# Kernel tuning notes

Hardware: AMD Instinct MI355X
Metric: run time of the kernel (lower is better)

## Reference

```python
import jax, jax.numpy as jnp
import numpy as np

N = 50000      # nodes
E = 400000     # edges (before self-loops)
IN = 128       # input feature dim
HID = 32       # out_channels per head
HEADS = 12
NC = 2         # num_classes
SLOPE = 0.2    # GATv2 leaky_relu negative slope


def setup_inputs() -> dict:
    key = jax.random.key(0)
    ks = jax.random.split(key, 24)
    f32 = jnp.float32
    def nrm(k, shape, s=0.1):
        return jax.random.normal(k, shape, dtype=f32) * s
    inp = {}
    inp["x"] = jax.random.normal(ks[0], (N, IN), dtype=f32)
    inp["edge_index"] = jax.random.randint(ks[1], (2, E), 0, N, dtype=jnp.int32)
    # GATv2 layer 0: in=IN, layer 1: in=HID; both heads=HEADS, out=HID, concat=False
    dims = [IN, HID]
    i = 2
    for l, d in enumerate(dims):
        inp[f"Wl{l}"] = nrm(ks[i], (d, HEADS * HID)); i += 1
        inp[f"bl{l}"] = jnp.zeros((HEADS * HID,), f32)
        inp[f"Wr{l}"] = nrm(ks[i], (d, HEADS * HID)); i += 1
        inp[f"br{l}"] = jnp.zeros((HEADS * HID,), f32)
        inp[f"att{l}"] = nrm(ks[i], (HEADS, HID)); i += 1
        inp[f"bias{l}"] = jnp.zeros((HID,), f32)
    # output GATv2Conv(HID, NC): heads=1, concat=True
    inp["Wlo"] = nrm(ks[i], (HID, NC)); i += 1
    inp["blo"] = jnp.zeros((NC,), f32)
    inp["Wro"] = nrm(ks[i], (HID, NC)); i += 1
    inp["bro"] = jnp.zeros((NC,), f32)
    inp["atto"] = nrm(ks[i], (1, NC)); i += 1
    inp["biaso"] = jnp.zeros((NC,), f32)
    return inp


def gatv2_conv(x, src, dst, Wl, bl, Wr, br, att, bias, heads, out_ch, concat):
    """PyG GATv2Conv (share_weights=False, self-loops pre-appended, eval mode)."""
    n = x.shape[0]
    xl = (x @ Wl + bl).reshape(n, heads, out_ch)   # source transform
    xr = (x @ Wr + br).reshape(n, heads, out_ch)   # target transform
    # per-edge attention: e_ij = att . leaky_relu(xl_j + xr_i)
    h = jax.nn.leaky_relu(xl[src] + xr[dst], SLOPE)            # [E, H, C]
    logits = jnp.einsum('ehc,hc->eh', h, att)                   # [E, H]
    # segment softmax over incoming edges per destination node
    m = jax.ops.segment_max(logits, dst, num_segments=n)        # [N, H]
    a = jnp.exp(logits - m[dst])
    denom = jax.ops.segment_sum(a, dst, num_segments=n)         # [N, H]
    alpha = a / (denom[dst] + 1e-16)                            # [E, H]
    out = jax.ops.segment_sum(xl[src] * alpha[..., None], dst, num_segments=n)
    out = out.reshape(n, heads * out_ch) if concat else out.mean(axis=1)
    return out + bias


def reference(x, edge_index, Wl0, bl0, Wr0, br0, att0, bias0,
              Wl1, bl1, Wr1, br1, att1, bias1,
              Wlo, blo, Wro, bro, atto, biaso):
    n = x.shape[0]
    loop = jnp.arange(n, dtype=edge_index.dtype)
    src = jnp.concatenate([edge_index[0], loop])  # add self-loops (PyG default)
    dst = jnp.concatenate([edge_index[1], loop])
    h = gatv2_conv(x, src, dst, Wl0, bl0, Wr0, br0, att0, bias0, HEADS, HID, False)
    h = jax.nn.elu(h)
    h = gatv2_conv(h, src, dst, Wl1, bl1, Wr1, br1, att1, bias1, HEADS, HID, False)
    h = jax.nn.elu(h)
    out = gatv2_conv(h, src, dst, Wlo, blo, Wro, bro, atto, biaso, 1, NC, True)
    return out
```

## Files before the change

kernel.cpp:

```cpp
#include <hip/hip_runtime.h>
#include <hip/hip_fp16.h>
#include <math.h>

#define IN_DIM 128
#define HID 32
#define HEADS 12
#define FDIM (HEADS*HID)
#define SLOPE 0.2f

typedef __attribute__((ext_vector_type(8))) short short8;
typedef __attribute__((ext_vector_type(4))) float float4v;
typedef __attribute__((ext_vector_type(4))) float f32x4;
typedef _Float16 hv2 __attribute__((ext_vector_type(2)));

__device__ __forceinline__ float dot2acc(hv2 a, hv2 b, float c) {
#if __has_builtin(__builtin_amdgcn_fdot2)
    return __builtin_amdgcn_fdot2(a, b, c, false);
#else
    return c + (float)a.x * (float)b.x + (float)a.y * (float)b.y;
#endif
}


__global__ void hist_kernel(const int* __restrict__ dst, int* __restrict__ cnt, int E) {
    int e = blockIdx.x * blockDim.x + threadIdx.x;
    if (e < E) atomicAdd(&cnt[dst[e]], 1);
}

__global__ __launch_bounds__(256) void scan_partial_kernel(const int* __restrict__ cnt,
                                                           int* __restrict__ partials, int n) {
    int i = blockIdx.x * 256 + threadIdx.x;
    int v = (i < n) ? cnt[i] : 0;
#pragma unroll
    for (int off = 1; off < 64; off <<= 1) v += __shfl_xor(v, off);
    __shared__ int sh[4];
    if ((threadIdx.x & 63) == 0) sh[threadIdx.x >> 6] = v;
    __syncthreads();
    if (threadIdx.x == 0) partials[blockIdx.x] = sh[0] + sh[1] + sh[2] + sh[3];
}

__global__ __launch_bounds__(1024) void scan_top_kernel(int* __restrict__ partials, int nb) {
    __shared__ int sh[1024];
    int t = threadIdx.x;
    int v = (t < nb) ? partials[t] : 0;
    sh[t] = v;
    __syncthreads();
    for (int off = 1; off < 1024; off <<= 1) {
        int u = (t >= off) ? sh[t - off] : 0;
        __syncthreads();
        sh[t] += u;
        __syncthreads();
    }
    if (t < nb) partials[t] = sh[t] - v;
}

__global__ __launch_bounds__(256) void scan_final_kernel(const int* __restrict__ cnt,
                                                         const int* __restrict__ partials,
                                                         int* __restrict__ start,
                                                         int* __restrict__ cursor, int n) {
    __shared__ int sh[256];
    int t = threadIdx.x;
    int i = blockIdx.x * 256 + t;
    int v = (i < n) ? cnt[i] : 0;
    sh[t] = v;
    __syncthreads();
    for (int off = 1; off < 256; off <<= 1) {
        int u = (t >= off) ? sh[t - off] : 0;
        __syncthreads();
        sh[t] += u;
        __syncthreads();
    }
    int ex = sh[t] - v + partials[blockIdx.x];
    if (i < n) {
        start[i] = ex;
        cursor[i] = ex;
        if (i == n - 1) start[n] = ex + v;
    }
}

__global__ void scatter_kernel(const int* __restrict__ src, const int* __restrict__ dst,
                               int* __restrict__ cursor, int* __restrict__ srcs,
                               int* __restrict__ srcsOff, int E) {
    int e = blockIdx.x * blockDim.x + threadIdx.x;
    if (e < E) {
        int d = dst[e];
        int pos = atomicAdd(&cursor[d], 1);
        int s = src[e];
        srcs[pos] = s;
        srcsOff[pos] = s * (FDIM * 2);
    }
}


__device__ __forceinline__ unsigned int bf16_rne(float f) {
    unsigned int u = __float_as_uint(f);
    return (u + 0x7FFFu + ((u >> 16) & 1u)) >> 16;
}


__global__ void prep_all(const float* __restrict__ Wl0, const float* __restrict__ Wr0,
                         const float* __restrict__ Wl1, const float* __restrict__ Wr1,
                         const float* __restrict__ a0, const float* __restrict__ a1,
                         short* __restrict__ Bl0h, short* __restrict__ Bl0l,
                         short* __restrict__ Br0h, short* __restrict__ Br0l,
                         short* __restrict__ Bl1h, short* __restrict__ Bl1l,
                         short* __restrict__ Br1h, short* __restrict__ Br1l,
                         _Float16* __restrict__ attH) {
    int idx = blockIdx.x * 256 + threadIdx.x;
    if (idx < 49152) {
        int k = idx / 384, n = idx - k * 384;
        float w1 = Wl0[idx], w2 = Wr0[idx];
        unsigned int h1 = bf16_rne(w1);
        unsigned int l1 = bf16_rne(w1 - __uint_as_float(h1 << 16));
        unsigned int h2 = bf16_rne(w2);
        unsigned int l2 = bf16_rne(w2 - __uint_as_float(h2 << 16));
        Bl0h[n * 128 + k] = (short)h1;  Bl0l[n * 128 + k] = (short)l1;
        Br0h[n * 128 + k] = (short)h2;  Br0l[n * 128 + k] = (short)l2;
    } else if (idx < 61440) {
        int i2 = idx - 49152;
        int k = i2 / 384, n = i2 - k * 384;
        float w1 = Wl1[i2], w2 = Wr1[i2];
        unsigned int h1 = bf16_rne(w1);
        unsigned int l1 = bf16_rne(w1 - __uint_as_float(h1 << 16));
        unsigned int h2 = bf16_rne(w2);
        unsigned int l2 = bf16_rne(w2 - __uint_as_float(h2 << 16));
        Bl1h[n * 32 + k] = (short)h1;  Bl1l[n * 32 + k] = (short)l1;
        Br1h[n * 32 + k] = (short)h2;  Br1l[n * 32 + k] = (short)l2;
    } else if (idx < 62208) {
        int i2 = idx - 61440;
        attH[i2] = (_Float16)((i2 < 384) ? a0[i2] : a1[i2 - 384]);
    }
}


__global__ void conv_x_kernel(const float* __restrict__ A, short* __restrict__ Ah,
                              short* __restrict__ Al, int total4) {
    int i = blockIdx.x * 256 + threadIdx.x;
    if (i >= total4) return;
    float4 v = ((const float4*)A)[i];
    float fs[4] = {v.x, v.y, v.z, v.w};
    unsigned int hb[4], lb[4];
#pragma unroll
    for (int t = 0; t < 4; t++) {
        hb[t] = bf16_rne(fs[t]);
        lb[t] = bf16_rne(fs[t] - __uint_as_float(hb[t] << 16));
    }
    uint2 hp, lp;
    hp.x = hb[0] | (hb[1] << 16); hp.y = hb[2] | (hb[3] << 16);
    lp.x = lb[0] | (lb[1] << 16); lp.y = lb[2] | (lb[3] << 16);
    ((uint2*)Ah)[i] = hp;
    ((uint2*)Al)[i] = lp;
}


__global__ __launch_bounds__(256) void gemm_pair_direct(
    const short* __restrict__ Ahi, const short* __restrict__ Alo,
    const short* __restrict__ B1h, const short* __restrict__ B1l,
    const float* __restrict__ bias1, __half* __restrict__ C1,
    const short* __restrict__ B2h, const short* __restrict__ B2l,
    const float* __restrict__ bias2, __half* __restrict__ C2,
    int M, int K) {
    __shared__ __align__(16) float Ct[64 * 132];
    int tid = threadIdx.x;
    int lane = tid & 63;
    int wave = tid >> 6;
    int wm = wave & 1, wn = wave >> 1;
    int rowBase = blockIdx.x * 128;
    bool second = blockIdx.y >= 3;
    int colBase = (blockIdx.y - (second ? 3 : 0)) * 128;
    const short* Bh  = second ? B2h : B1h;
    const short* Bl  = second ? B2l : B1l;
    const float* bias = second ? bias2 : bias1;
    __half*      C    = second ? C2 : C1;

    int fr = lane & 15;
    int fo = (lane >> 4) << 3;

    float4v acc[4][4];
#pragma unroll
    for (int i = 0; i < 4; i++)
#pragma unroll
        for (int j = 0; j < 4; j++) acc[i][j] = (float4v){0.f, 0.f, 0.f, 0.f};

    const short* Ar = Ahi + (long)(rowBase + wm * 64 + fr) * K + fo;
    const short* Al_ = Alo + (long)(rowBase + wm * 64 + fr) * K + fo;
    const short* Br_ = Bh + (long)(colBase + wn * 64 + fr) * K + fo;
    const short* Bl_ = Bl + (long)(colBase + wn * 64 + fr) * K + fo;
    long rstep = (long)16 * K;

    for (int kt = 0; kt < K; kt += 32) {
        short8 ah[4], al[4], bh[4], blv[4];
#pragma unroll
        for (int i = 0; i < 4; i++) {
            ah[i]  = *(const short8*)(Ar  + i * rstep + kt);
            al[i]  = *(const short8*)(Al_ + i * rstep + kt);
            bh[i]  = *(const short8*)(Br_ + i * rstep + kt);
            blv[i] = *(const short8*)(Bl_ + i * rstep + kt);
        }
#pragma unroll
        for (int i = 0; i < 4; i++)
#pragma unroll
            for (int j = 0; j < 4; j++) {
                acc[i][j] = __builtin_amdgcn_mfma_f32_16x16x32_bf16(ah[i], bh[j],  acc[i][j], 0, 0, 0);
                acc[i][j] = __builtin_amdgcn_mfma_f32_16x16x32_bf16(ah[i], blv[j], acc[i][j], 0, 0, 0);
                acc[i][j] = __builtin_amdgcn_mfma_f32_16x16x32_bf16(al[i], bh[j],  acc[i][j], 0, 0, 0);
            }
    }

    int cq = lane >> 4, cn = lane & 15;
#pragma unroll
    for (int ph = 0; ph < 2; ph++) {
        __syncthreads();
        if (wm == ph) {
#pragma unroll
            for (int i = 0; i < 4; i++)
#pragma unroll
                for (int j = 0; j < 4; j++) {
                    int lr = i * 16 + cq * 4;
                    int lc = wn * 64 + j * 16 + cn;
#pragma unroll
                    for (int r = 0; r < 4; r++)
                        Ct[(lr + r) * 132 + lc] = acc[i][j][r];
                }
        }
        __syncthreads();
#pragma unroll
        for (int k = 0; k < 4; k++) {
            int o = k * 256 + tid;
            int lr = o >> 4;
            int oc = (o & 15) << 3;
            int gr = rowBase + ph * 64 + lr;
            if (gr < M) {
                float4 f0 = *(float4*)&Ct[lr * 132 + oc];
                float4 f1 = *(float4*)&Ct[lr * 132 + oc + 4];
                int gc = colBase + oc;
                float4 b0 = *(const float4*)(bias + gc);
                float4 b1 = *(const float4*)(bias + gc + 4);
                __half2 p0 = __floats2half2_rn(f0.x + b0.x, f0.y + b0.y);
                __half2 p1 = __floats2half2_rn(f0.z + b0.z, f0.w + b0.w);
                __half2 p2 = __floats2half2_rn(f1.x + b1.x, f1.y + b1.y);
                __half2 p3 = __floats2half2_rn(f1.z + b1.z, f1.w + b1.w);
                uint4 ov;
                ov.x = *(unsigned int*)&p0;
                ov.y = *(unsigned int*)&p1;
                ov.z = *(unsigned int*)&p2;
                ov.w = *(unsigned int*)&p3;
                *(uint4*)(C + (size_t)gr * FDIM + gc) = ov;
            }
        }
    }
}


__global__ __launch_bounds__(64) void agg_kernel(const __half* __restrict__ xl,
                                                 const __half* __restrict__ xr,
                                                 const _Float16* __restrict__ att_h,
                                                 const float* __restrict__ bias,
                                                 const int* __restrict__ start,
                                                 const int* __restrict__ srcsOff,
                                                 short* __restrict__ houtHi,
                                                 short* __restrict__ houtLo,
                                                 const float* __restrict__ Wl,
                                                 const float* __restrict__ bl,
                                                 const float* __restrict__ Wr,
                                                 const float* __restrict__ br,
                                                 float* __restrict__ xloB,
                                                 float* __restrict__ xroB, int N) {
    int node = blockIdx.x;
    if (node >= N) return;
    int lane = threadIdx.x & 63;
    int hl = lane & 31;
    int half_ = lane >> 5;
    int cb = hl << 3;

    long nodeOff = (long)node * (FDIM * 2);
    hv2 xr2[6], at2[6];
    f32x4 acc[3];
    float s[3];
#pragma unroll
    for (int c = 0; c < 3; c++) {
        uint2 ur = *(const uint2*)((const char*)xr + nodeOff + c * 256 + cb);
        xr2[2*c]   = __builtin_bit_cast(hv2, ur.x);
        xr2[2*c+1] = __builtin_bit_cast(hv2, ur.y);
        uint2 ua = *(const uint2*)((const char*)att_h + c * 256 + cb);
        at2[2*c]   = __builtin_bit_cast(hv2, ua.x);
        at2[2*c+1] = __builtin_bit_cast(hv2, ua.y);
        acc[c] = (f32x4){0.f, 0.f, 0.f, 0.f};
        s[c] = 0.f;
    }
    const hv2 sl2 = {(_Float16)SLOPE, (_Float16)SLOPE};
    const char* xlb = (const char*)xl;

    int e0 = start[node], e1 = start[node + 1];

    for (int b = e0 - 1; b < e1; b += 4) {
        hv2 xa[2][6];
        float mask[2];
#pragma unroll
        for (int p = 0; p < 2; p++) {
            int myIdx = b + p * 2 + half_;
            int ic = min(myIdx, e1 - 1);
            long off = (ic < e0) ? nodeOff : (long)srcsOff[ic];
            mask[p] = (myIdx < e1) ? 0.f : -1e30f;
            const char* base = xlb + off + cb;
            uint2 u0 = *(const uint2*)(base);
            uint2 u1 = *(const uint2*)(base + 256);
            uint2 u2 = *(const uint2*)(base + 512);
            xa[p][0] = __builtin_bit_cast(hv2, u0.x); xa[p][1] = __builtin_bit_cast(hv2, u0.y);
            xa[p][2] = __builtin_bit_cast(hv2, u1.x); xa[p][3] = __builtin_bit_cast(hv2, u1.y);
            xa[p][4] = __builtin_bit_cast(hv2, u2.x); xa[p][5] = __builtin_bit_cast(hv2, u2.y);
        }
#pragma unroll
        for (int p = 0; p < 2; p++) {
            float pc[3];
#pragma unroll
            for (int c = 0; c < 3; c++) {
                hv2 t0 = xa[p][2*c]   + xr2[2*c];
                hv2 t1 = xa[p][2*c+1] + xr2[2*c+1];
                t0 = __builtin_elementwise_max(t0, t0 * sl2);
                t1 = __builtin_elementwise_max(t1, t1 * sl2);
                pc[c] = dot2acc(t1, at2[2*c+1], dot2acc(t0, at2[2*c], 0.f));
            }
#pragma unroll
            for (int st = 1; st <= 4; st <<= 1) {
                pc[0] += __shfl_xor(pc[0], st);
                pc[1] += __shfl_xor(pc[1], st);
                pc[2] += __shfl_xor(pc[2], st);
            }
#pragma unroll
            for (int c = 0; c < 3; c++) {
                float a = __expf(pc[c] + mask[p]);
                s[c] += a;
                acc[c].x = fmaf(a, (float)xa[p][2*c].x,   acc[c].x);
                acc[c].y = fmaf(a, (float)xa[p][2*c].y,   acc[c].y);
                acc[c].z = fmaf(a, (float)xa[p][2*c+1].x, acc[c].z);
                acc[c].w = fmaf(a, (float)xa[p][2*c+1].y, acc[c].w);
            }
        }
    }

#pragma unroll
    for (int c = 0; c < 3; c++) {
        acc[c].x += __shfl_xor(acc[c].x, 32);
        acc[c].y += __shfl_xor(acc[c].y, 32);
        acc[c].z += __shfl_xor(acc[c].z, 32);
        acc[c].w += __shfl_xor(acc[c].w, 32);
        s[c] += __shfl_xor(s[c], 32);
    }
    f32x4 v[3];
#pragma unroll
    for (int c = 0; c < 3; c++) {
        float inv = 1.f / (s[c] + 1e-16f);
        f32x4 iv = {inv, inv, inv, inv};
        v[c] = acc[c] * iv;
    }
#pragma unroll
    for (int st = 8; st <= 16; st <<= 1) {
#pragma unroll
        for (int c = 0; c < 3; c++) {
            v[c].x += __shfl_xor(v[c].x, st);
            v[c].y += __shfl_xor(v[c].y, st);
            v[c].z += __shfl_xor(v[c].z, st);
            v[c].w += __shfl_xor(v[c].w, st);
        }
    }
    if (lane < 8) {
        f32x4 b4 = *(const f32x4*)(bias + (hl << 2));
        f32x4 o = (v[0] + v[1] + v[2]) * (f32x4){1.f/12.f, 1.f/12.f, 1.f/12.f, 1.f/12.f} + b4;
        o.x = o.x > 0.f ? o.x : expm1f(o.x);
        o.y = o.y > 0.f ? o.y : expm1f(o.y);
        o.z = o.z > 0.f ? o.z : expm1f(o.z);
        o.w = o.w > 0.f ? o.w : expm1f(o.w);
        if (houtHi) {
            float fs[4] = {o.x, o.y, o.z, o.w};
            unsigned int hb[4], lb[4];
#pragma unroll
            for (int t = 0; t < 4; t++) {
                hb[t] = bf16_rne(fs[t]);
                lb[t] = bf16_rne(fs[t] - __uint_as_float(hb[t] << 16));
            }
            uint2 hp, lp;
            hp.x = hb[0] | (hb[1] << 16); hp.y = hb[2] | (hb[3] << 16);
            lp.x = lb[0] | (lb[1] << 16); lp.y = lb[2] | (lb[3] << 16);
            *(uint2*)(houtHi + (size_t)node * 32 + (hl << 2)) = hp;
            *(uint2*)(houtLo + (size_t)node * 32 + (hl << 2)) = lp;
        }
        if (Wl) {
            f32x4 wl0 = *(const f32x4*)(Wl + (hl << 3));
            f32x4 wl1 = *(const f32x4*)(Wl + (hl << 3) + 4);
            f32x4 wr0 = *(const f32x4*)(Wr + (hl << 3));
            f32x4 wr1 = *(const f32x4*)(Wr + (hl << 3) + 4);
            float l0 = o.x * wl0.x + o.y * wl0.z + o.z * wl1.x + o.w * wl1.z;
            float l1 = o.x * wl0.y + o.y * wl0.w + o.z * wl1.y + o.w * wl1.w;
            float r0 = o.x * wr0.x + o.y * wr0.z + o.z * wr1.x + o.w * wr1.z;
            float r1 = o.x * wr0.y + o.y * wr0.w + o.z * wr1.y + o.w * wr1.w;
#pragma unroll
            for (int st = 1; st <= 4; st <<= 1) {
                l0 += __shfl_xor(l0, st); l1 += __shfl_xor(l1, st);
                r0 += __shfl_xor(r0, st); r1 += __shfl_xor(r1, st);
            }
            if (hl == 0) {
                xloB[2 * node]     = l0 + bl[0];
                xloB[2 * node + 1] = l1 + bl[1];
                xroB[2 * node]     = r0 + br[0];
                xroB[2 * node + 1] = r1 + br[1];
            }
        }
    }
}


__global__ void out_agg_kernel(const float* __restrict__ xlo, const float* __restrict__ xro,
                               const float* __restrict__ atto, const float* __restrict__ biaso,
                               const int* __restrict__ start, const int* __restrict__ srcs,
                               float* __restrict__ out, int N) {
    int i = blockIdx.x * blockDim.x + threadIdx.x;
    if (i >= N) return;
    float a0 = atto[0], a1 = atto[1];
    float xr0 = xro[2 * i], xr1 = xro[2 * i + 1];
    float s = 0.f, acc0 = 0.f, acc1 = 0.f;
    int e0 = start[i], e1 = start[i + 1];
    for (int idx = e0 - 1; idx < e1; ++idx) {
        int j = (idx < e0) ? i : srcs[idx];
        float x0 = xlo[2 * j], x1 = xlo[2 * j + 1];
        float t0 = x0 + xr0, t1 = x1 + xr1;
        t0 = fmaxf(t0, SLOPE * t0);
        t1 = fmaxf(t1, SLOPE * t1);
        float L = a0 * t0 + a1 * t1;
        float a = __expf(L);
        s += a;
        acc0 = fmaf(a, x0, acc0);
        acc1 = fmaf(a, x1, acc1);
    }
    float inv = 1.0f / (s + 1e-16f);
    out[2 * i]     = acc0 * inv + biaso[0];
    out[2 * i + 1] = acc1 * inv + biaso[1];
}


extern "C" void kernel_launch(void* const* d_in, const int* in_sizes, int n_in,
                              void* d_out, int out_size, void* d_ws, size_t ws_size,
                              hipStream_t stream) {
    const float* x    = (const float*)d_in[0];
    const int*   ei   = (const int*)d_in[1];
    const float* Wl0  = (const float*)d_in[2];
    const float* bl0  = (const float*)d_in[3];
    const float* Wr0  = (const float*)d_in[4];
    const float* br0  = (const float*)d_in[5];
    const float* att0 = (const float*)d_in[6];
    const float* bias0= (const float*)d_in[7];
    const float* Wl1  = (const float*)d_in[8];
    const float* bl1  = (const float*)d_in[9];
    const float* Wr1  = (const float*)d_in[10];
    const float* br1  = (const float*)d_in[11];
    const float* att1 = (const float*)d_in[12];
    const float* bias1= (const float*)d_in[13];
    const float* Wlo  = (const float*)d_in[14];
    const float* blo  = (const float*)d_in[15];
    const float* Wro  = (const float*)d_in[16];
    const float* bro  = (const float*)d_in[17];
    const float* atto = (const float*)d_in[18];
    const float* biaso= (const float*)d_in[19];

    const int N = in_sizes[0] / IN_DIM;
    const int E = in_sizes[1] / 2;

    char* ws = (char*)d_ws;
    size_t off = 0;
    auto take = [&](size_t bytes) -> char* {
        char* p = ws + off;
        off += (bytes + 255) & ~(size_t)255;
        return p;
    };
    __half* xlf = (__half*)take((size_t)N * FDIM * 2);
    __half* xrf = (__half*)take((size_t)N * FDIM * 2);
    float* xloB = (float*)take((size_t)N * 2 * 4);
    float* xroB = (float*)take((size_t)N * 2 * 4);
    int* cnt    = (int*)take((size_t)N * 4);
    int* startA = (int*)take((size_t)(N + 1) * 4);
    int* cursor = (int*)take((size_t)N * 4);
    int* srcs   = (int*)take((size_t)E * 4);
    int* srcsOff= (int*)take((size_t)E * 4);
    int  nb     = (N + 255) / 256;
    int* partials = (int*)take((size_t)nb * 4);
    short* Bl0h = (short*)take((size_t)FDIM * IN_DIM * 2);
    short* Bl0l = (short*)take((size_t)FDIM * IN_DIM * 2);
    short* Br0h = (short*)take((size_t)FDIM * IN_DIM * 2);
    short* Br0l = (short*)take((size_t)FDIM * IN_DIM * 2);
    short* Bl1h = (short*)take((size_t)FDIM * HID * 2);
    short* Bl1l = (short*)take((size_t)FDIM * HID * 2);
    short* Br1h = (short*)take((size_t)FDIM * HID * 2);
    short* Br1l = (short*)take((size_t)FDIM * HID * 2);
    short* xh   = (short*)take((size_t)N * IN_DIM * 2);
    short* xlo_ = (short*)take((size_t)N * IN_DIM * 2);
    short* h0h  = (short*)take((size_t)N * HID * 2);
    short* h0l  = (short*)take((size_t)N * HID * 2);
    _Float16* attH = (_Float16*)take((size_t)768 * 2);
    (void)take(16384);

    const int* esrc = ei;
    const int* edst = ei + E;

    prep_all<<<(62208 + 255) / 256, 256, 0, stream>>>(Wl0, Wr0, Wl1, Wr1, att0, att1,
                                                      Bl0h, Bl0l, Br0h, Br0l,
                                                      Bl1h, Bl1l, Br1h, Br1l, attH);
    conv_x_kernel<<<((N * IN_DIM / 4) + 255) / 256, 256, 0, stream>>>(x, xh, xlo_, N * IN_DIM / 4);

    hipMemsetAsync(cnt, 0, (size_t)N * 4, stream);
    hist_kernel<<<(E + 255) / 256, 256, 0, stream>>>(edst, cnt, E);
    scan_partial_kernel<<<nb, 256, 0, stream>>>(cnt, partials, N);
    scan_top_kernel<<<1, 1024, 0, stream>>>(partials, nb);
    scan_final_kernel<<<nb, 256, 0, stream>>>(cnt, partials, startA, cursor, N);
    scatter_kernel<<<(E + 255) / 256, 256, 0, stream>>>(esrc, edst, cursor, srcs, srcsOff, E);

    dim3 ggrid((N + 127) / 128, 6);
    gemm_pair_direct<<<ggrid, 256, 0, stream>>>(xh, xlo_, Bl0h, Bl0l, bl0, xlf, Br0h, Br0l, br0, xrf, N, IN_DIM);
    agg_kernel<<<N, 64, 0, stream>>>(xlf, xrf, attH, bias0, startA, srcsOff,
                                     h0h, h0l, nullptr, nullptr, nullptr, nullptr,
                                     nullptr, nullptr, N);
    gemm_pair_direct<<<ggrid, 256, 0, stream>>>(h0h, h0l, Bl1h, Bl1l, bl1, xlf, Br1h, Br1l, br1, xrf, N, HID);
    agg_kernel<<<N, 64, 0, stream>>>(xlf, xrf, attH + 384, bias1, startA, srcsOff,
                                     nullptr, nullptr, Wlo, blo, Wro, bro,
                                     xloB, xroB, N);
    out_agg_kernel<<<(N + 255) / 256, 256, 0, stream>>>(xloB, xroB, atto, biaso, startA, srcs, (float*)d_out, N);
}
```

Before: 422.1 us.

## Stage GEMM tiles through LDS with register-prefetched double buffering

The split-bf16 GEMM now loads A and B tiles cooperatively into LDS in an MFMA-fragment-friendly layout instead of each wave reading its fragments straight from global memory. The next K-slice is prefetched into registers while the current slice is computed, overlapping global latency with MFMA work. It also bounds-checks A rows and drops the padding allocation in the workspace. The cost is extra LDS traffic and two barriers per K step. GEMMs are only part of total time, which is dominated by the aggregation kernels.

```diff
diff --git a/kernel.cpp b/kernel.cpp
--- a/kernel.cpp
+++ b/kernel.cpp
@@ -153,14 +153,18 @@
 }
 
 
-__global__ __launch_bounds__(256) void gemm_pair_direct(
+__global__ __launch_bounds__(256) void gemm_pair_mfma_db(
     const short* __restrict__ Ahi, const short* __restrict__ Alo,
     const short* __restrict__ B1h, const short* __restrict__ B1l,
     const float* __restrict__ bias1, __half* __restrict__ C1,
     const short* __restrict__ B2h, const short* __restrict__ B2l,
     const float* __restrict__ bias2, __half* __restrict__ C2,
     int M, int K) {
-    __shared__ __align__(16) float Ct[64 * 132];
+    __shared__ __align__(16) unsigned char smem[33792];
+    uint4* AsHi = (uint4*)smem;
+    uint4* AsLo = AsHi + 512;
+    uint4* BsHi = AsLo + 512;
+    uint4* BsLo = BsHi + 512;
     int tid = threadIdx.x;
     int lane = tid & 63;
     int wave = tid >> 6;
@@ -173,8 +177,21 @@
     const float* bias = second ? bias2 : bias1;
     __half*      C    = second ? C2 : C1;
 
-    int fr = lane & 15;
-    int fo = (lane >> 4) << 3;
+    int cA0 = tid,        oA0 = cA0 >> 7, rA0 = cA0 & 127;
+    int cA1 = 256 + tid,  oA1 = cA1 >> 7, rA1 = cA1 & 127;
+    int sA0 = (rA0 >> 4) * 64 + (oA0 << 4) + (rA0 & 15);
+    int sA1 = (rA1 >> 4) * 64 + (oA1 << 4) + (rA1 & 15);
+    bool vA0 = rowBase + rA0 < M, vA1 = rowBase + rA1 < M;
+    long aOff0 = (long)(rowBase + rA0) * K + oA0 * 8;
+    long aOff1 = (long)(rowBase + rA1) * K + oA1 * 8;
+    int sB[4]; long bOff[4];
+#pragma unroll
+    for (int i = 0; i < 4; i++) {
+        int c = i * 256 + tid;
+        int o = (c >> 7) & 3, n = c & 127;
+        sB[i] = (n >> 4) * 64 + (o << 4) + (n & 15);
+        bOff[i] = (long)(colBase + n) * K + o * 8;
+    }
 
     float4v acc[4][4];
 #pragma unroll
@@ -182,20 +199,43 @@
 #pragma unroll
         for (int j = 0; j < 4; j++) acc[i][j] = (float4v){0.f, 0.f, 0.f, 0.f};
 
-    const short* Ar = Ahi + (long)(rowBase + wm * 64 + fr) * K + fo;
-    const short* Al_ = Alo + (long)(rowBase + wm * 64 + fr) * K + fo;
-    const short* Br_ = Bh + (long)(colBase + wn * 64 + fr) * K + fo;
-    const short* Bl_ = Bl + (long)(colBase + wn * 64 + fr) * K + fo;
-    long rstep = (long)16 * K;
+    uint4 z4 = make_uint4(0, 0, 0, 0);
+    uint4 pA0h, pA0l, pA1h, pA1l, pB[4];
+    pA0h = vA0 ? *(const uint4*)(Ahi + aOff0) : z4;
+    pA0l = vA0 ? *(const uint4*)(Alo + aOff0) : z4;
+    pA1h = vA1 ? *(const uint4*)(Ahi + aOff1) : z4;
+    pA1l = vA1 ? *(const uint4*)(Alo + aOff1) : z4;
+    pB[0] = *(const uint4*)(Bh + bOff[0]);
+    pB[1] = *(const uint4*)(Bh + bOff[1]);
+    pB[2] = *(const uint4*)(Bl + bOff[2]);
+    pB[3] = *(const uint4*)(Bl + bOff[3]);
 
     for (int kt = 0; kt < K; kt += 32) {
+        AsHi[sA0] = pA0h; AsLo[sA0] = pA0l;
+        AsHi[sA1] = pA1h; AsLo[sA1] = pA1l;
+        BsHi[sB[0]] = pB[0]; BsHi[sB[1]] = pB[1];
+        BsLo[sB[2]] = pB[2]; BsLo[sB[3]] = pB[3];
+        __syncthreads();
+
+        int kn = kt + 32;
+        if (kn < K) {
+            pA0h = vA0 ? *(const uint4*)(Ahi + aOff0 + kn) : z4;
+            pA0l = vA0 ? *(const uint4*)(Alo + aOff0 + kn) : z4;
+            pA1h = vA1 ? *(const uint4*)(Ahi + aOff1 + kn) : z4;
+            pA1l = vA1 ? *(const uint4*)(Alo + aOff1 + kn) : z4;
+            pB[0] = *(const uint4*)(Bh + bOff[0] + kn);
+            pB[1] = *(const uint4*)(Bh + bOff[1] + kn);
+            pB[2] = *(const uint4*)(Bl + bOff[2] + kn);
+            pB[3] = *(const uint4*)(Bl + bOff[3] + kn);
+        }
+
         short8 ah[4], al[4], bh[4], blv[4];
 #pragma unroll
         for (int i = 0; i < 4; i++) {
-            ah[i]  = *(const short8*)(Ar  + i * rstep + kt);
-            al[i]  = *(const short8*)(Al_ + i * rstep + kt);
-            bh[i]  = *(const short8*)(Br_ + i * rstep + kt);
-            blv[i] = *(const short8*)(Bl_ + i * rstep + kt);
+            ah[i]  = ((const short8*)AsHi)[(wm * 4 + i) * 64 + lane];
+            al[i]  = ((const short8*)AsLo)[(wm * 4 + i) * 64 + lane];
+            bh[i]  = ((const short8*)BsHi)[(wn * 4 + i) * 64 + lane];
+            blv[i] = ((const short8*)BsLo)[(wn * 4 + i) * 64 + lane];
         }
 #pragma unroll
         for (int i = 0; i < 4; i++)
@@ -205,12 +245,13 @@
                 acc[i][j] = __builtin_amdgcn_mfma_f32_16x16x32_bf16(ah[i], blv[j], acc[i][j], 0, 0, 0);
                 acc[i][j] = __builtin_amdgcn_mfma_f32_16x16x32_bf16(al[i], bh[j],  acc[i][j], 0, 0, 0);
             }
-    }
-
+        __syncthreads();
+    }
+
+    float* Ct = (float*)smem;
     int cq = lane >> 4, cn = lane & 15;
 #pragma unroll
     for (int ph = 0; ph < 2; ph++) {
-        __syncthreads();
         if (wm == ph) {
 #pragma unroll
             for (int i = 0; i < 4; i++)
@@ -248,6 +289,7 @@
                 *(uint4*)(C + (size_t)gr * FDIM + gc) = ov;
             }
         }
+        __syncthreads();
     }
 }
 
@@ -496,7 +538,6 @@
     short* h0h  = (short*)take((size_t)N * HID * 2);
     short* h0l  = (short*)take((size_t)N * HID * 2);
     _Float16* attH = (_Float16*)take((size_t)768 * 2);
-    (void)take(16384);
 
     const int* esrc = ei;
     const int* edst = ei + E;
@@ -514,11 +555,11 @@
     scatter_kernel<<<(E + 255) / 256, 256, 0, stream>>>(esrc, edst, cursor, srcs, srcsOff, E);
 
     dim3 ggrid((N + 127) / 128, 6);
-    gemm_pair_direct<<<ggrid, 256, 0, stream>>>(xh, xlo_, Bl0h, Bl0l, bl0, xlf, Br0h, Br0l, br0, xrf, N, IN_DIM);
+    gemm_pair_mfma_db<<<ggrid, 256, 0, stream>>>(xh, xlo_, Bl0h, Bl0l, bl0, xlf, Br0h, Br0l, br0, xrf, N, IN_DIM);
     agg_kernel<<<N, 64, 0, stream>>>(xlf, xrf, attH, bias0, startA, srcsOff,
                                      h0h, h0l, nullptr, nullptr, nullptr, nullptr,
                                      nullptr, nullptr, N);
-    gemm_pair_direct<<<ggrid, 256, 0, stream>>>(h0h, h0l, Bl1h, Bl1l, bl1, xlf, Br1h, Br1l, br1, xrf, N, HID);
+    gemm_pair_mfma_db<<<ggrid, 256, 0, stream>>>(h0h, h0l, Bl1h, Bl1l, bl1, xlf, Br1h, Br1l, br1, xrf, N, HID);
     agg_kernel<<<N, 64, 0, stream>>>(xlf, xrf, attH + 384, bias1, startA, srcsOff,
                                      nullptr, nullptr, Wlo, blo, Wro, bro,
                                      xloB, xroB, N);
```

After: 435.0 us. 1.03x slower.

## Stage GEMM tiles via async global-to-LDS loads and parallelize output aggregation

Applied to the files above, without the earlier changes.

The bf16x3 GEMM now loads its A and B hi/lo tiles into shared memory with global_load_lds 16-byte async copies and reads MFMA fragments from LDS. Each fragment is now fetched from global memory once per block instead of once per wave. This adds two barriers per K step and has no double buffering. Separately, the final one-head output aggregation uses 8 lanes per node with a shuffle reduction instead of one thread per node, which shortens the serial edge loop for high-degree nodes.

```diff
diff --git a/kernel.cpp b/kernel.cpp
--- a/kernel.cpp
+++ b/kernel.cpp
@@ -19,6 +19,12 @@
 #else
     return c + (float)a.x * (float)b.x + (float)a.y * (float)b.y;
 #endif
+}
+
+__device__ __forceinline__ void async_cp16(const void* g, void* l) {
+    __builtin_amdgcn_global_load_lds(
+        (const __attribute__((address_space(1))) void*)g,
+        (__attribute__((address_space(3))) void*)l, 16, 0, 0);
 }
 
 
@@ -153,14 +159,14 @@
 }
 
 
-__global__ __launch_bounds__(256) void gemm_pair_direct(
+__global__ __launch_bounds__(256) void gemm_pair_async(
     const short* __restrict__ Ahi, const short* __restrict__ Alo,
     const short* __restrict__ B1h, const short* __restrict__ B1l,
     const float* __restrict__ bias1, __half* __restrict__ C1,
     const short* __restrict__ B2h, const short* __restrict__ B2l,
     const float* __restrict__ bias2, __half* __restrict__ C2,
     int M, int K) {
-    __shared__ __align__(16) float Ct[64 * 132];
+    __shared__ __align__(16) unsigned char smem[33792];
     int tid = threadIdx.x;
     int lane = tid & 63;
     int wave = tid >> 6;
@@ -173,8 +179,23 @@
     const float* bias = second ? bias2 : bias1;
     __half*      C    = second ? C2 : C1;
 
-    int fr = lane & 15;
-    int fo = (lane >> 4) << 3;
+    const short8* AsHi = (const short8*)smem;
+    const short8* AsLo = (const short8*)(smem + 8192);
+    const short8* BsHi = (const short8*)(smem + 16384);
+    const short8* BsLo = (const short8*)(smem + 24576);
+
+    const short* gsrc[8];
+    void* ldst[8];
+#pragma unroll
+    for (int q = 0; q < 8; q++) {
+        int t  = (q & 1) * 4 + wave;
+        int rc = t * 16 + (lane & 15);
+        int ko = (lane >> 4) * 8;
+        const short* base = (q < 2) ? Ahi : (q < 4) ? Alo : (q < 6) ? Bh : Bl;
+        int rb = (q < 4) ? rowBase : colBase;
+        gsrc[q] = base + (long)(rb + rc) * K + ko;
+        ldst[q] = (void*)(smem + q * 4096 + wave * 1024);
+    }
 
     float4v acc[4][4];
 #pragma unroll
@@ -182,20 +203,21 @@
 #pragma unroll
         for (int j = 0; j < 4; j++) acc[i][j] = (float4v){0.f, 0.f, 0.f, 0.f};
 
-    const short* Ar = Ahi + (long)(rowBase + wm * 64 + fr) * K + fo;
-    const short* Al_ = Alo + (long)(rowBase + wm * 64 + fr) * K + fo;
-    const short* Br_ = Bh + (long)(colBase + wn * 64 + fr) * K + fo;
-    const short* Bl_ = Bl + (long)(colBase + wn * 64 + fr) * K + fo;
-    long rstep = (long)16 * K;
-
     for (int kt = 0; kt < K; kt += 32) {
+#pragma unroll
+        for (int q = 0; q < 8; q++) {
+            async_cp16(gsrc[q], ldst[q]);
+            gsrc[q] += 32;
+        }
+        __syncthreads();
+
         short8 ah[4], al[4], bh[4], blv[4];
 #pragma unroll
         for (int i = 0; i < 4; i++) {
-            ah[i]  = *(const short8*)(Ar  + i * rstep + kt);
-            al[i]  = *(const short8*)(Al_ + i * rstep + kt);
-            bh[i]  = *(const short8*)(Br_ + i * rstep + kt);
-            blv[i] = *(const short8*)(Bl_ + i * rstep + kt);
+            ah[i]  = AsHi[(wm * 4 + i) * 64 + lane];
+            al[i]  = AsLo[(wm * 4 + i) * 64 + lane];
+            bh[i]  = BsHi[(wn * 4 + i) * 64 + lane];
+            blv[i] = BsLo[(wn * 4 + i) * 64 + lane];
         }
 #pragma unroll
         for (int i = 0; i < 4; i++)
@@ -205,12 +227,13 @@
                 acc[i][j] = __builtin_amdgcn_mfma_f32_16x16x32_bf16(ah[i], blv[j], acc[i][j], 0, 0, 0);
                 acc[i][j] = __builtin_amdgcn_mfma_f32_16x16x32_bf16(al[i], bh[j],  acc[i][j], 0, 0, 0);
             }
-    }
-
+        __syncthreads();
+    }
+
+    float* Ct = (float*)smem;
     int cq = lane >> 4, cn = lane & 15;
 #pragma unroll
     for (int ph = 0; ph < 2; ph++) {
-        __syncthreads();
         if (wm == ph) {
 #pragma unroll
             for (int i = 0; i < 4; i++)
@@ -248,6 +271,7 @@
                 *(uint4*)(C + (size_t)gr * FDIM + gc) = ov;
             }
         }
+        __syncthreads();
     }
 }
 
@@ -410,19 +434,23 @@
 }
 
 
-__global__ void out_agg_kernel(const float* __restrict__ xlo, const float* __restrict__ xro,
-                               const float* __restrict__ atto, const float* __restrict__ biaso,
-                               const int* __restrict__ start, const int* __restrict__ srcs,
-                               float* __restrict__ out, int N) {
-    int i = blockIdx.x * blockDim.x + threadIdx.x;
-    if (i >= N) return;
+__global__ __launch_bounds__(256) void out_agg_kernel(const float* __restrict__ xlo,
+                                                      const float* __restrict__ xro,
+                                                      const float* __restrict__ atto,
+                                                      const float* __restrict__ biaso,
+                                                      const int* __restrict__ start,
+                                                      const int* __restrict__ srcs,
+                                                      float* __restrict__ out, int N) {
+    int g = (blockIdx.x * blockDim.x + threadIdx.x) >> 3;
+    int j = threadIdx.x & 7;
+    if (g >= N) return;
     float a0 = atto[0], a1 = atto[1];
-    float xr0 = xro[2 * i], xr1 = xro[2 * i + 1];
+    float xr0 = xro[2 * g], xr1 = xro[2 * g + 1];
     float s = 0.f, acc0 = 0.f, acc1 = 0.f;
-    int e0 = start[i], e1 = start[i + 1];
-    for (int idx = e0 - 1; idx < e1; ++idx) {
-        int j = (idx < e0) ? i : srcs[idx];
-        float x0 = xlo[2 * j], x1 = xlo[2 * j + 1];
+    int e0 = start[g], e1 = start[g + 1];
+    for (int idx = e0 - 1 + j; idx < e1; idx += 8) {
+        int jj = (idx < e0) ? g : srcs[idx];
+        float x0 = xlo[2 * jj], x1 = xlo[2 * jj + 1];
         float t0 = x0 + xr0, t1 = x1 + xr1;
         t0 = fmaxf(t0, SLOPE * t0);
         t1 = fmaxf(t1, SLOPE * t1);
@@ -432,9 +460,17 @@
         acc0 = fmaf(a, x0, acc0);
         acc1 = fmaf(a, x1, acc1);
     }
-    float inv = 1.0f / (s + 1e-16f);
-    out[2 * i]     = acc0 * inv + biaso[0];
-    out[2 * i + 1] = acc1 * inv + biaso[1];
+#pragma unroll
+    for (int st = 1; st <= 4; st <<= 1) {
+        s    += __shfl_xor(s, st);
+        acc0 += __shfl_xor(acc0, st);
+        acc1 += __shfl_xor(acc1, st);
+    }
+    if (j == 0) {
+        float inv = 1.0f / (s + 1e-16f);
+        out[2 * g]     = acc0 * inv + biaso[0];
+        out[2 * g + 1] = acc1 * inv + biaso[1];
+    }
 }
 
 
@@ -496,7 +532,7 @@
     short* h0h  = (short*)take((size_t)N * HID * 2);
     short* h0l  = (short*)take((size_t)N * HID * 2);
     _Float16* attH = (_Float16*)take((size_t)768 * 2);
-    (void)take(16384);
+    (void)take(32768);
 
     const int* esrc = ei;
     const int* edst = ei + E;
@@ -514,13 +550,13 @@
     scatter_kernel<<<(E + 255) / 256, 256, 0, stream>>>(esrc, edst, cursor, srcs, srcsOff, E);
 
     dim3 ggrid((N + 127) / 128, 6);
-    gemm_pair_direct<<<ggrid, 256, 0, stream>>>(xh, xlo_, Bl0h, Bl0l, bl0, xlf, Br0h, Br0l, br0, xrf, N, IN_DIM);
+    gemm_pair_async<<<ggrid, 256, 0, stream>>>(xh, xlo_, Bl0h, Bl0l, bl0, xlf, Br0h, Br0l, br0, xrf, N, IN_DIM);
     agg_kernel<<<N, 64, 0, stream>>>(xlf, xrf, attH, bias0, startA, srcsOff,
                                      h0h, h0l, nullptr, nullptr, nullptr, nullptr,
                                      nullptr, nullptr, N);
-    gemm_pair_direct<<<ggrid, 256, 0, stream>>>(h0h, h0l, Bl1h, Bl1l, bl1, xlf, Br1h, Br1l, br1, xrf, N, HID);
+    gemm_pair_async<<<ggrid, 256, 0, stream>>>(h0h, h0l, Bl1h, Bl1l, bl1, xlf, Br1h, Br1l, br1, xrf, N, HID);
     agg_kernel<<<N, 64, 0, stream>>>(xlf, xrf, attH + 384, bias1, startA, srcsOff,
                                      nullptr, nullptr, Wlo, blo, Wro, bro,
                                      xloB, xroB, N);
-    out_agg_kernel<<<(N + 255) / 256, 256, 0, stream>>>(xloB, xroB, atto, biaso, startA, srcs, (float*)d_out, N);
-}
+    out_agg_kernel<<<((size_t)N * 8 + 255) / 256, 256, 0, stream>>>(xloB, xroB, atto, biaso, startA, srcs, (float*)d_out, N);
+}
```

After: 385.0 us, median of 2. -8.8%, faster.
